# Kernel tuning notes

Hardware: AMD Instinct MI355X
Metric: run time of the kernel (lower is better)

The kernel has to match this reference:

```python
import jax, jax.numpy as jnp
import numpy as np

T, S, B = 8192, 1024, 8192


def setup_inputs() -> dict:
    key = jax.random.key(0)
    k1, k2, k3, k4, k5, k6 = jax.random.split(key, 6)
    return {
        "t": jax.random.randint(k1, (B,), 0, T),
        "s": jax.random.randint(k2, (B,), 0, S),
        "obs": jax.random.randint(k3, (T, S), 0, 5).astype(jnp.int32),
        "alpha": jax.random.uniform(k4, (S, S), dtype=jnp.float32),
        "beta": jax.random.uniform(k5, (1,), jnp.float32, 0.1, 1.0),
        "mu": jax.random.uniform(k6, (S,), dtype=jnp.float32),
    }


def reference(t, s, obs, alpha, beta, mu):
    # lam(t,s) = relu( mu[s] + beta * sum_{tp<t, sp} alpha[sp,s]*obs[tp,sp]*exp(-beta*(t-tp)) )
    # Exact rewrite of the O(T^2*S) brute force:
    #   c[tp, s] = sum_sp obs[tp, sp] * alpha[sp, s]          (GEMM)
    #   H[t, s]  = sum_{tp<t} c[tp, s] * exp(-beta*(t-tp))    (linear recurrence)
    obs_f = obs.astype(alpha.dtype)
    c = obs_f @ alpha                      # [T, S]
    a = jnp.exp(-beta[0])                  # per-step decay

    def step(h, c_t):
        h = a * (h + c_t)                  # H[t] = a*(H[t-1] + c[t-1])
        return h, h

    _, H_tail = jax.lax.scan(step, jnp.zeros_like(c[0]), c[:-1])  # H[1..T-1]
    H = jnp.concatenate([jnp.zeros_like(c[:1]), H_tail], axis=0)  # [T, S], H[0]=0

    lam_grid = jax.nn.relu(mu[None, :] + beta[0] * H)  # [T, S]
    return lam_grid[t, s]                  # [B]
```

## Files before the change

kernel.cpp:

```cpp
#include <hip/hip_runtime.h>
#include <hip/hip_bf16.h>
#include <stdint.h>

#define T_DIM 8192
#define S_DIM 1024
#define B_DIM 8192
#define CHUNK 64
#define NCHUNK 128
#define QCAP 2048
#define PASS_ROWS 8
#define NPASS 8

#define OFF_ALPHAT 0u
#define OFF_OBS8   4194304u
#define WS_NEEDED  12582912u

__global__ void pack_obs_kernel(const int* __restrict__ obs,
                                unsigned char* __restrict__ obs8) {
    int i = (blockIdx.x * 256 + threadIdx.x) * 16;
    uint32_t w[4];
    #pragma unroll
    for (int g = 0; g < 4; ++g) {
        int4 v = *(const int4*)(obs + i + g * 4);
        w[g] = (uint32_t)v.x | ((uint32_t)v.y << 8)
             | ((uint32_t)v.z << 16) | ((uint32_t)v.w << 24);
    }
    uint4 o; o.x = w[0]; o.y = w[1]; o.z = w[2]; o.w = w[3];
    *(uint4*)(obs8 + i) = o;
}

__global__ void transpose_alpha_kernel(const float* __restrict__ alpha,
                                       float* __restrict__ alphaT) {
    __shared__ float tile[32][33];
    int bx = blockIdx.x * 32;
    int by = blockIdx.y * 32;
    int tx = threadIdx.x, ty = threadIdx.y;
    #pragma unroll
    for (int j = 0; j < 32; j += 8)
        tile[ty + j][tx] = alpha[(size_t)(by + ty + j) * S_DIM + bx + tx];
    __syncthreads();
    #pragma unroll
    for (int j = 0; j < 32; j += 8)
        alphaT[(size_t)(bx + ty + j) * S_DIM + by + tx] = tile[tx][ty + j];
}

__global__ __launch_bounds__(1024, 1) void hawkes_kernel(
        const int* __restrict__ tq, const int* __restrict__ sq,
        const unsigned char* __restrict__ obs8,
        const float* __restrict__ beta, const float* __restrict__ mu,
        const float* __restrict__ alphaT,
        float* __restrict__ out) {
    const int k    = blockIdx.x;
    const int tid  = threadIdx.x;
    const int wv   = tid >> 6, lane = tid & 63;
    const float b  = beta[0];
    const float a  = expf(-b);
    const int  t0  = k << 6;

    __shared__ int   qtmp[QCAP];
    __shared__ int   qcnt_s;
    __shared__ float Gall[PASS_ROWS][S_DIM];

    if (tid == 0) qcnt_s = 0;
    __syncthreads();

    for (int i = tid; i < B_DIM; i += 1024) {
        int tv = tq[i];
        if ((tv >> 6) == k) {
            int p = atomicAdd(&qcnt_s, 1);
            if (p < QCAP) qtmp[p] = ((tv - t0) << 13) | i;
        }
    }

    int Dmax = ((int)(26.0f / b) + 4 + 3) & ~3;
    const int n  = t0 < Dmax ? t0 : Dmax;
    const int ts = t0 - n;
    const int Q4 = n >> 2;

    const int m  = tid >> 8;
    const int c4 = (tid & 255) << 2;
    float A4 = a * a; A4 = A4 * A4;
    float F0 = 0.f, F1 = 0.f, F2 = 0.f, F3 = 0.f;
    const unsigned char* obase = obs8 + (size_t)(ts + m) * S_DIM + c4;

    int q = 0;
    for (; q + 8 <= Q4; q += 8) {
        uint32_t o[8];
        #pragma unroll
        for (int r = 0; r < 8; ++r)
            o[r] = *(const uint32_t*)(obase + (size_t)(q + r) * 4 * S_DIM);
        #pragma unroll
        for (int r = 0; r < 8; ++r) {
            F0 = A4 * (F0 + (float)( o[r]        & 0xFF));
            F1 = A4 * (F1 + (float)((o[r] >>  8) & 0xFF));
            F2 = A4 * (F2 + (float)((o[r] >> 16) & 0xFF));
            F3 = A4 * (F3 + (float)( o[r] >> 24));
        }
    }
    for (; q < Q4; ++q) {
        uint32_t ov = *(const uint32_t*)(obase + (size_t)q * 4 * S_DIM);
        F0 = A4 * (F0 + (float)( ov        & 0xFF));
        F1 = A4 * (F1 + (float)((ov >>  8) & 0xFF));
        F2 = A4 * (F2 + (float)((ov >> 16) & 0xFF));
        F3 = A4 * (F3 + (float)( ov >> 24));
    }
    float inva = 1.f / a;
    float am = (m == 0) ? 1.f : (m == 1) ? inva
             : (m == 2) ? inva * inva : inva * inva * inva;
    float4 cw; cw.x = F0 * am; cw.y = F1 * am; cw.z = F2 * am; cw.w = F3 * am;
    __syncthreads();
    *(float4*)&Gall[m][c4] = cw;
    __syncthreads();
    float U = Gall[0][tid] + Gall[1][tid] + Gall[2][tid] + Gall[3][tid];
    __syncthreads();
    const int Q = qcnt_s < QCAP ? qcnt_s : QCAP;

    float G = U;
    for (int pass = 0; pass < NPASS; ++pass) {
        const int jlo = pass * PASS_ROWS;
        unsigned char o[PASS_ROWS];
        #pragma unroll
        for (int r = 0; r < PASS_ROWS; ++r)
            o[r] = obs8[(size_t)(t0 + jlo + r) * S_DIM + tid];
        #pragma unroll
        for (int r = 0; r < PASS_ROWS; ++r) {
            Gall[r][tid] = G;
            G = a * (G + (float)o[r]);
        }
        __syncthreads();
        for (int p = wv; p < Q; p += 16) {
            int key = qtmp[p];
            int j = key >> 13;
            if (j < jlo || j >= jlo + PASS_ROWS) continue;
            int i = key & 8191;
            int s = sq[i];
            const float* ar = alphaT + (size_t)s * S_DIM;
            const float* gr = &Gall[j - jlo][0];
            float acc = 0.f;
            #pragma unroll
            for (int cc = 0; cc < 4; ++cc) {
                float4 gv = *(const float4*)(gr + 256 * cc + lane * 4);
                float4 av = *(const float4*)(ar + 256 * cc + lane * 4);
                acc += gv.x * av.x + gv.y * av.y + gv.z * av.z + gv.w * av.w;
            }
            #pragma unroll
            for (int off = 32; off > 0; off >>= 1)
                acc += __shfl_down(acc, off);
            if (lane == 0) {
                float lam = mu[s] + b * acc;
                out[i] = lam > 0.f ? lam : 0.f;
            }
        }
        __syncthreads();
    }
}

__global__ __launch_bounds__(1024) void chunk_all_kernel(
        const int* __restrict__ tq, const int* __restrict__ sq,
        const int* __restrict__ obs, const float* __restrict__ alpha,
        const float* __restrict__ beta, const float* __restrict__ mu,
        float* __restrict__ out) {
    const int k   = blockIdx.x;
    const int tid = threadIdx.x;
    const float b = beta[0];
    const float a = expf(-b);
    const int t0 = k << 6;
    __shared__ int   qkey[2048];
    __shared__ int   qcnt_s;
    __shared__ float wred[16];
    if (tid == 0) qcnt_s = 0;
    __syncthreads();
    for (int i = tid; i < B_DIM; i += 1024) {
        int tv = tq[i];
        if ((tv >> 6) == k) {
            int p = atomicAdd(&qcnt_s, 1);
            if (p < 2048) qkey[p] = ((tv - t0) << 13) | i;
        }
    }
    __syncthreads();
    int Q = qcnt_s; if (Q > 2048) Q = 2048;
    float G = 0.f;
    for (int tp = 0; tp < t0; tp += 8) {
        int o[8];
        #pragma unroll
        for (int r = 0; r < 8; ++r) o[r] = obs[(size_t)(tp + r) * S_DIM + tid];
        #pragma unroll
        for (int r = 0; r < 8; ++r) G = a * (G + (float)o[r]);
    }
    for (int j = 0; j < 64; ++j) {
        for (int q = 0; q < Q; ++q) {
            int key = qkey[q];
            if ((key >> 13) == j) {
                int i = key & 8191;
                int s = sq[i];
                float p = G * alpha[(size_t)tid * S_DIM + s];
                #pragma unroll
                for (int off = 32; off > 0; off >>= 1) p += __shfl_down(p, off);
                if ((tid & 63) == 0) wred[tid >> 6] = p;
                __syncthreads();
                if (tid < 64) {
                    float v = (tid < 16) ? wred[tid] : 0.f;
                    v += __shfl_down(v, 8); v += __shfl_down(v, 4);
                    v += __shfl_down(v, 2); v += __shfl_down(v, 1);
                    if (tid == 0) {
                        float lam = mu[s] + b * v;
                        out[i] = lam > 0.f ? lam : 0.f;
                    }
                }
                __syncthreads();
            }
        }
        int o = obs[(size_t)(t0 + j) * S_DIM + tid];
        G = a * (G + (float)o);
    }
}

extern "C" void kernel_launch(void* const* d_in, const int* in_sizes, int n_in,
                              void* d_out, int out_size, void* d_ws, size_t ws_size,
                              hipStream_t stream) {
    const int*   t     = (const int*)d_in[0];
    const int*   s     = (const int*)d_in[1];
    const int*   obs   = (const int*)d_in[2];
    const float* alpha = (const float*)d_in[3];
    const float* beta  = (const float*)d_in[4];
    const float* mu    = (const float*)d_in[5];
    float* out = (float*)d_out;

    if (ws_size < (size_t)WS_NEEDED || d_ws == nullptr) {
        chunk_all_kernel<<<128, 1024, 0, stream>>>(t, s, obs, alpha, beta, mu, out);
        return;
    }

    char* ws = (char*)d_ws;
    float*         alphaT = (float*)(ws + OFF_ALPHAT);
    unsigned char* obs8   = (unsigned char*)(ws + OFF_OBS8);

    pack_obs_kernel<<<T_DIM * S_DIM / (256 * 16), 256, 0, stream>>>(obs, obs8);
    transpose_alpha_kernel<<<dim3(32, 32), dim3(32, 8), 0, stream>>>(alpha, alphaT);
    hawkes_kernel<<<NCHUNK, 1024, 0, stream>>>(t, s, obs8, beta, mu, alphaT, out);
}
```

Measured before the change: 120.0 us.

## Halve time chunk size to 256 blocks and fuse obs packing with alpha transpose

Time chunks shrink from 64 to 32 rows, so the main kernel launches 256 blocks instead of 128. This fills more of the GPU's compute units and gives each block a shorter serial recurrence and fewer queries. Block indices are permuted, likely to spread neighbouring time chunks across XCDs. The obs int8 packing and the alpha transpose now share one prep kernel, saving one launch. In exchange, every block repeats the t-index scan over all queries, and the geometric prefix warm-up is computed twice as often.

```diff
diff --git a/kernel.cpp b/kernel.cpp
--- a/kernel.cpp
+++ b/kernel.cpp
@@ -5,43 +5,45 @@
 #define T_DIM 8192
 #define S_DIM 1024
 #define B_DIM 8192
-#define CHUNK 64
-#define NCHUNK 128
-#define QCAP 2048
+#define CHUNK 32
+#define NCHUNK 256
+#define QCAP 1024
 #define PASS_ROWS 8
-#define NPASS 8
+#define NPASS 4
 
 #define OFF_ALPHAT 0u
 #define OFF_OBS8   4194304u
 #define WS_NEEDED  12582912u
 
-__global__ void pack_obs_kernel(const int* __restrict__ obs,
-                                unsigned char* __restrict__ obs8) {
-    int i = (blockIdx.x * 256 + threadIdx.x) * 16;
-    uint32_t w[4];
+__global__ __launch_bounds__(1024) void prep_kernel(
+        const int* __restrict__ obs, const float* __restrict__ alpha,
+        unsigned char* __restrict__ obs8, float* __restrict__ alphaT) {
+    const int tid = threadIdx.x;
+    int base = (blockIdx.x * 1024 + tid) * 32;
     #pragma unroll
-    for (int g = 0; g < 4; ++g) {
-        int4 v = *(const int4*)(obs + i + g * 4);
-        w[g] = (uint32_t)v.x | ((uint32_t)v.y << 8)
-             | ((uint32_t)v.z << 16) | ((uint32_t)v.w << 24);
-    }
-    uint4 o; o.x = w[0]; o.y = w[1]; o.z = w[2]; o.w = w[3];
-    *(uint4*)(obs8 + i) = o;
-}
-
-__global__ void transpose_alpha_kernel(const float* __restrict__ alpha,
-                                       float* __restrict__ alphaT) {
+    for (int g = 0; g < 2; ++g) {
+        uint32_t w[4];
+        #pragma unroll
+        for (int h = 0; h < 4; ++h) {
+            int4 v = *(const int4*)(obs + base + g * 16 + h * 4);
+            w[h] = (uint32_t)v.x | ((uint32_t)v.y << 8)
+                 | ((uint32_t)v.z << 16) | ((uint32_t)v.w << 24);
+        }
+        uint4 o; o.x = w[0]; o.y = w[1]; o.z = w[2]; o.w = w[3];
+        *(uint4*)(obs8 + base + g * 16) = o;
+    }
     __shared__ float tile[32][33];
-    int bx = blockIdx.x * 32;
-    int by = blockIdx.y * 32;
-    int tx = threadIdx.x, ty = threadIdx.y;
+    const int ty = tid >> 5, tx = tid & 31;
     #pragma unroll
-    for (int j = 0; j < 32; j += 8)
-        tile[ty + j][tx] = alpha[(size_t)(by + ty + j) * S_DIM + bx + tx];
-    __syncthreads();
-    #pragma unroll
-    for (int j = 0; j < 32; j += 8)
-        alphaT[(size_t)(bx + ty + j) * S_DIM + by + tx] = tile[tx][ty + j];
+    for (int rep = 0; rep < 4; ++rep) {
+        int tile_id = blockIdx.x * 4 + rep;
+        int by = (tile_id >> 5) << 5;
+        int bx = (tile_id & 31) << 5;
+        __syncthreads();
+        tile[ty][tx] = alpha[(size_t)(by + ty) * S_DIM + bx + tx];
+        __syncthreads();
+        alphaT[(size_t)(bx + ty) * S_DIM + by + tx] = tile[tx][ty];
+    }
 }
 
 __global__ __launch_bounds__(1024, 1) void hawkes_kernel(
@@ -50,12 +52,12 @@
         const float* __restrict__ beta, const float* __restrict__ mu,
         const float* __restrict__ alphaT,
         float* __restrict__ out) {
-    const int k    = blockIdx.x;
+    const int k    = ((blockIdx.x & 7) << 5) | (blockIdx.x >> 3);
     const int tid  = threadIdx.x;
     const int wv   = tid >> 6, lane = tid & 63;
     const float b  = beta[0];
     const float a  = expf(-b);
-    const int  t0  = k << 6;
+    const int  t0  = k << 5;
 
     __shared__ int   qtmp[QCAP];
     __shared__ int   qcnt_s;
@@ -66,7 +68,7 @@
 
     for (int i = tid; i < B_DIM; i += 1024) {
         int tv = tq[i];
-        if ((tv >> 6) == k) {
+        if ((tv >> 5) == k) {
             int p = atomicAdd(&qcnt_s, 1);
             if (p < QCAP) qtmp[p] = ((tv - t0) << 13) | i;
         }
@@ -235,7 +237,6 @@
     float*         alphaT = (float*)(ws + OFF_ALPHAT);
     unsigned char* obs8   = (unsigned char*)(ws + OFF_OBS8);
 
-    pack_obs_kernel<<<T_DIM * S_DIM / (256 * 16), 256, 0, stream>>>(obs, obs8);
-    transpose_alpha_kernel<<<dim3(32, 32), dim3(32, 8), 0, stream>>>(alpha, alphaT);
+    prep_kernel<<<NCHUNK, 1024, 0, stream>>>(obs, alpha, obs8, alphaT);
     hawkes_kernel<<<NCHUNK, 1024, 0, stream>>>(t, s, obs8, beta, mu, alphaT, out);
 }
```

New measurement: 107.9 us. 10.1% less time.
